# Performance work log

Measured on AMD Instinct MI355X. Metric: run time of the kernel, lower is better.

## Reference

```python
import jax, jax.numpy as jnp
import numpy as np

N_NODES = 100000
N_EDGES = 1600000
F_IN = 128
EMB = 128
HEADS = 4
D_HEAD = EMB // HEADS
HIDDEN = 256
BATCH = 2048
CANDS = 16  # distractors + 1


def setup_inputs() -> dict:
    key = jax.random.key(0)
    ks = jax.random.split(key, 10)
    message = jax.random.normal(ks[0], (BATCH, HIDDEN), jnp.float32)
    x = jax.random.normal(ks[1], (N_NODES, F_IN), jnp.float32)
    edge_index = jax.random.randint(ks[2], (2, N_EDGES), 0, N_NODES, jnp.int64)
    indices = jax.random.randint(ks[3], (BATCH * CANDS,), 0, N_NODES, jnp.int64)
    s = 1.0 / np.sqrt(F_IN)
    W = jax.random.normal(ks[4], (F_IN, HEADS, D_HEAD), jnp.float32) * s
    att_src = jax.random.normal(ks[5], (HEADS, D_HEAD), jnp.float32) * s
    att_dst = jax.random.normal(ks[6], (HEADS, D_HEAD), jnp.float32) * s
    bias = jnp.zeros((EMB,), jnp.float32)
    fc_w = jax.random.normal(ks[7], (EMB, HIDDEN), jnp.float32) / np.sqrt(HIDDEN)
    fc_b = jnp.zeros((EMB,), jnp.float32)
    return {"message": message, "x": x, "edge_index": edge_index, "indices": indices,
            "W": W, "att_src": att_src, "att_dst": att_dst, "bias": bias,
            "fc_w": fc_w, "fc_b": fc_b}


def _gat(x, edge_index, W, att_src, att_dst, bias):
    N = x.shape[0]
    loops = jnp.arange(N, dtype=edge_index.dtype)
    src = jnp.concatenate([edge_index[0], loops])  # self-loops (PyG default)
    dst = jnp.concatenate([edge_index[1], loops])
    Wx = jnp.einsum('nf,fhd->nhd', x, W)                      # [N,H,D]
    a_s = (Wx * att_src).sum(-1)                              # [N,H]
    a_d = (Wx * att_dst).sum(-1)
    e = jax.nn.leaky_relu(a_s[src] + a_d[dst], 0.2)           # [E,H]
    m = jax.ops.segment_max(e, dst, num_segments=N)           # segment softmax
    ex = jnp.exp(e - m[dst])
    den = jax.ops.segment_sum(ex, dst, num_segments=N)
    alpha = ex / den[dst]
    out = jax.ops.segment_sum(alpha[:, :, None] * Wx[src], dst, num_segments=N)
    return out.reshape(N, -1) + bias                          # [N, H*D]


def reference(message, x, edge_index, indices, W, att_src, att_dst, bias, fc_w, fc_b):
    h = _gat(x, edge_index, W, att_src, att_dst, bias)        # [N, EMB]
    B = message.shape[0]
    emb = h[indices].reshape(B, -1, h.shape[-1])              # [B,C,EMB]
    msg = message @ fc_w.T + fc_b                             # [B,EMB]
    dots = jnp.einsum('bce,be->bc', emb, msg)                 # bmm scoring
    amax = jnp.abs(dots).max()
    tie = ((jnp.abs(dots) - amax) < 1e-10).astype(dots.dtype)
    noise = jax.random.normal(jax.random.key(42), dots.shape, dots.dtype)
    dots = dots + tie * amax * 1e-5 * noise
    return jax.nn.log_softmax(dots, axis=1)
```

## Files before the change

### kernel.cpp

```cpp
#include <hip/hip_runtime.h>
#include <stdint.h>
#include <stddef.h>

#define N_NODES 100000
#define N_EDGES 1600000
#define F_IN 128
#define EMB 128
#define HEADS 4
#define D_HEAD 32
#define HIDDEN 256
#define BATCH 2048
#define CANDS 16
#define NSLOTS 32768
#define WTROWS 144
#define STR 136

#define WX_BLOCKS 782
#define MSG_BLOCKS 256
#define EDGE_QUADS 400000
#define EDGE_BLOCKS 1563
#define MEGA_BLOCKS 2610

typedef __attribute__((ext_vector_type(8))) short v8s;
typedef __attribute__((ext_vector_type(4))) float v4f;

__device__ __forceinline__ unsigned short f2bs(float f) {
  unsigned int u = __builtin_bit_cast(unsigned int, f);
  u = (u + 0x7fffu + ((u >> 16) & 1u)) >> 16;
  return (unsigned short)u;
}
__device__ __forceinline__ float bs2f(unsigned int s) {
  unsigned int u = (s & 0xffffu) << 16;
  return __builtin_bit_cast(float, u);
}

__global__ __launch_bounds__(256) void k_prep(const float* __restrict__ W,
                                              const float* __restrict__ att_src,
                                              const float* __restrict__ att_dst,
                                              unsigned short* __restrict__ Wtp,
                                              const int* __restrict__ idx,
                                              int* __restrict__ nidx,
                                              int* __restrict__ cnt) {
  int i = blockIdx.x * 256 + threadIdx.x;
  if (i < 128 * STR) {
    int r = i / STR, c = i - r * STR;
    Wtp[i] = (c < 128) ? f2bs(W[c * 128 + r]) : (unsigned short)0;
  } else if (i < WTROWS * STR) {
    int ii = i - 128 * STR;
    int r = ii / STR, c = ii - r * STR;
    unsigned short v = 0;
    if (c < 128 && r < 8) {
      const float* att = (r < 4) ? att_src : att_dst;
      int hh = r & 3;
      float s = 0.f;
#pragma unroll
      for (int d = 0; d < 32; ++d) s += W[c * 128 + hh * 32 + d] * att[hh * 32 + d];
      v = f2bs(s);
    }
    Wtp[i] = v;
  }
  if (i < NSLOTS) {
    cnt[i] = 0;
    nidx[idx[i]] = i;
  }
}

__global__ __launch_bounds__(256) void k_mega(const float* __restrict__ x,
                                              const unsigned short* __restrict__ Wtp,
                                              unsigned short* __restrict__ Wx,
                                              float* __restrict__ a_s,
                                              float* __restrict__ a_d,
                                              const int* __restrict__ ei,
                                              const int* __restrict__ idx,
                                              const int* __restrict__ nidx,
                                              int* __restrict__ cnt,
                                              int* __restrict__ srclist,
                                              const float* __restrict__ message,
                                              const float* __restrict__ fc_w,
                                              const float* __restrict__ fc_b,
                                              float* __restrict__ msg) {
  __shared__ unsigned short smem[WTROWS * STR];
  int tid = threadIdx.x;
  int sub = blockIdx.x % 10, grp = blockIdx.x / 10;

  if (sub < 3) {
    int wxid = grp * 3 + sub;
    if (wxid >= WX_BLOCKS) return;
    unsigned short* wt = smem;
    {
      const uint4* s = (const uint4*)Wtp;
      uint4* d = (uint4*)wt;
#pragma unroll
      for (int it = 0; it < 10; ++it) {
        int i = it * 256 + tid;
        if (i < WTROWS * STR / 8) d[i] = s[i];
      }
    }
    __syncthreads();

    int w = tid >> 6, lane = tid & 63;
    int m = lane & 15, quad = lane >> 4;

    for (int chunk = 0; chunk < 2; ++chunk) {
      int rbase = wxid * 128 + chunk * 64;
      int gr = rbase + w * 16 + m;
      if (gr >= N_NODES) gr = N_NODES - 1;
      const float* xrow = x + (size_t)gr * 128;

      v8s afrag[4];
#pragma unroll
      for (int t = 0; t < 4; ++t) {
        const float4* gp = (const float4*)(xrow + t * 32 + quad * 8);
        float4 f0 = gp[0], f1 = gp[1];
        v8s a;
        a[0] = (short)f2bs(f0.x); a[1] = (short)f2bs(f0.y);
        a[2] = (short)f2bs(f0.z); a[3] = (short)f2bs(f0.w);
        a[4] = (short)f2bs(f1.x); a[5] = (short)f2bs(f1.y);
        a[6] = (short)f2bs(f1.z); a[7] = (short)f2bs(f1.w);
        afrag[t] = a;
      }

      v4f acc[9];
#pragma unroll
      for (int nt = 0; nt < 9; ++nt) {
        v4f a0 = {0.f, 0.f, 0.f, 0.f};
        const unsigned short* brow = wt + (size_t)(nt * 16 + m) * STR;
#pragma unroll
        for (int t = 0; t < 4; ++t) {
          v8s b = *(const v8s*)(brow + t * 32 + quad * 8);
          a0 = __builtin_amdgcn_mfma_f32_16x16x32_bf16(afrag[t], b, a0, 0, 0, 0);
        }
        acc[nt] = a0;
      }

#pragma unroll
      for (int r = 0; r < 4; ++r) {
        int orow = rbase + w * 16 + quad * 4 + r;
        if (orow < N_NODES) {
          if (m < 4) a_s[(size_t)orow * 4 + m] = acc[8][r];
          else if (m < 8) a_d[(size_t)orow * 4 + m - 4] = acc[8][r];
          v8s v;
#pragma unroll
          for (int nt = 0; nt < 8; ++nt) v[nt] = (short)f2bs(acc[nt][r]);
          *(v8s*)(&Wx[(size_t)orow * 128 + m * 8]) = v;
        }
      }
    }
  } else if (sub == 3) {
    int msgid = grp;
    if (msgid >= MSG_BLOCKS) return;
    float* Sm = (float*)smem;
    float* red = ((float*)smem) + 2048;
    int b0 = msgid * 8;
    for (int i = tid; i < 8 * 256; i += 256)
      Sm[i] = message[(size_t)b0 * 256 + i];
    __syncthreads();
    int e = tid & 127, half = tid >> 7;
    float acc[8];
#pragma unroll
    for (int r = 0; r < 8; ++r) acc[r] = 0.f;
    const float* wrow = fc_w + (size_t)e * 256 + half * 128;
    for (int k = 0; k < 128; k += 4) {
      float4 w4 = *(const float4*)(wrow + k);
#pragma unroll
      for (int r = 0; r < 8; ++r) {
        float4 m4 = *(const float4*)(&Sm[r * 256 + half * 128 + k]);
        acc[r] += m4.x * w4.x + m4.y * w4.y + m4.z * w4.z + m4.w * w4.w;
      }
    }
    __syncthreads();
    if (half == 0) {
#pragma unroll
      for (int r = 0; r < 8; ++r) red[r * 128 + e] = acc[r];
    }
    __syncthreads();
    if (half == 1) {
#pragma unroll
      for (int r = 0; r < 8; ++r) red[r * 128 + e] += acc[r];
    }
    __syncthreads();
    for (int i = tid; i < 1024; i += 256)
      msg[(size_t)b0 * 128 + i] = red[i] + fc_b[i & 127];
  } else {
    int scid = grp * 6 + (sub - 4);
    if (scid >= EDGE_BLOCKS) return;
    int e4 = scid * 256 + tid;
    if (e4 >= EDGE_QUADS) return;
    int base = e4 * 4;
    int4 d4 = *(const int4*)(ei + N_EDGES + base);
    int4 s4 = *(const int4*)(ei + base);
    int dst[4] = {d4.x, d4.y, d4.z, d4.w};
    int src[4] = {s4.x, s4.y, s4.z, s4.w};
    unsigned int ni[4];
#pragma unroll
    for (int j = 0; j < 4; ++j) ni[j] = (unsigned int)nidx[dst[j]];
    bool ok[4];
#pragma unroll
    for (int j = 0; j < 4; ++j) {
      unsigned int c = ni[j] < NSLOTS ? ni[j] : 0u;
      ok[j] = (ni[j] < NSLOTS) && (idx[c] == dst[j]);
    }
#pragma unroll
    for (int j = 0; j < 4; ++j) {
      if (ok[j]) {
        int pos = atomicAdd(&cnt[ni[j]], 1);
        if (pos < 64) srclist[ni[j] * 64 + pos] = src[j];
      }
    }
  }
}

__global__ __launch_bounds__(256) void k_aggscore(const float* __restrict__ a_s,
                                                  const float* __restrict__ a_d,
                                                  const unsigned short* __restrict__ Wx,
                                                  const int* __restrict__ idx,
                                                  const int* __restrict__ nidx,
                                                  const int* __restrict__ cnt,
                                                  const int* __restrict__ srclist,
                                                  const int* __restrict__ ei,
                                                  const float* __restrict__ bias,
                                                  const float* __restrict__ msg,
                                                  float* __restrict__ out) {
  __shared__ int sS[16][64];
  __shared__ float sW[16][64 * 4];
  __shared__ float sdots[16];
  int w = threadIdx.x >> 6, lane = threadIdx.x & 63;
  int q = lane >> 4, li = lane & 15;
  int wq = w * 4 + q;
  int b = blockIdx.x;
  int wid = b * 16 + wq;
  int dst = idx[wid];
  int ci = nidx[dst];
  int degRaw = cnt[ci];
  int deg = degRaw < 64 ? degRaw : 64;
  float4 ad4 = *(const float4*)(a_d + (size_t)dst * 4);
  float4 dsum = {0.f, 0.f, 0.f, 0.f};
  for (int t = li; t < deg; t += 16) {
    int sv = srclist[ci * 64 + t];
    float4 as = *(const float4*)(a_s + (size_t)sv * 4);
    float e0 = as.x + ad4.x; e0 = e0 > 0.f ? e0 : 0.2f * e0;
    float e1 = as.y + ad4.y; e1 = e1 > 0.f ? e1 : 0.2f * e1;
    float e2 = as.z + ad4.z; e2 = e2 > 0.f ? e2 : 0.2f * e2;
    float e3 = as.w + ad4.w; e3 = e3 > 0.f ? e3 : 0.2f * e3;
    float4 w4;
    w4.x = __expf(e0); w4.y = __expf(e1);
    w4.z = __expf(e2); w4.w = __expf(e3);
    sS[wq][t] = sv;
    *(float4*)(&sW[wq][t * 4]) = w4;
    dsum.x += w4.x; dsum.y += w4.y; dsum.z += w4.z; dsum.w += w4.w;
  }
  asm volatile("s_waitcnt lgkmcnt(0)" ::: "memory");

#pragma unroll
  for (int o = 8; o >= 1; o >>= 1) {
    dsum.x += __shfl_xor(dsum.x, o);
    dsum.y += __shfl_xor(dsum.y, o);
    dsum.z += __shfl_xor(dsum.z, o);
    dsum.w += __shfl_xor(dsum.w, o);
  }

  float4 as4 = *(const float4*)(a_s + (size_t)dst * 4);
  float s0 = as4.x + ad4.x; s0 = s0 > 0.f ? s0 : 0.2f * s0;
  float s1 = as4.y + ad4.y; s1 = s1 > 0.f ? s1 : 0.2f * s1;
  float s2 = as4.z + ad4.z; s2 = s2 > 0.f ? s2 : 0.2f * s2;
  float s3 = as4.w + ad4.w; s3 = s3 > 0.f ? s3 : 0.2f * s3;
  float wself[4];
  wself[0] = __expf(s0); wself[1] = __expf(s1);
  wself[2] = __expf(s2); wself[3] = __expf(s3);
  float den4[4];
  den4[0] = dsum.x + wself[0]; den4[1] = dsum.y + wself[1];
  den4[2] = dsum.z + wself[2]; den4[3] = dsum.w + wself[3];

  float acc[8];
  {
    uint4 u = *(const uint4*)(Wx + (size_t)dst * 128 + li * 8);
    acc[0] = wself[0] * bs2f(u.x); acc[1] = wself[0] * bs2f(u.x >> 16);
    acc[2] = wself[1] * bs2f(u.y); acc[3] = wself[1] * bs2f(u.y >> 16);
    acc[4] = wself[2] * bs2f(u.z); acc[5] = wself[2] * bs2f(u.z >> 16);
    acc[6] = wself[3] * bs2f(u.w); acc[7] = wself[3] * bs2f(u.w >> 16);
  }

  if (degRaw > 64) {
    den4[0] = wself[0]; den4[1] = wself[1];
    den4[2] = wself[2]; den4[3] = wself[3];
    for (int e = 0; e < N_EDGES; ++e) {
      if (ei[N_EDGES + e] == dst) {
        int sv = ei[e];
        float4 as = *(const float4*)(a_s + (size_t)sv * 4);
        float e0 = as.x + ad4.x; e0 = e0 > 0.f ? e0 : 0.2f * e0;
        float e1 = as.y + ad4.y; e1 = e1 > 0.f ? e1 : 0.2f * e1;
        float e2 = as.z + ad4.z; e2 = e2 > 0.f ? e2 : 0.2f * e2;
        float e3 = as.w + ad4.w; e3 = e3 > 0.f ? e3 : 0.2f * e3;
        float wa0 = __expf(e0), wa1 = __expf(e1);
        float wa2 = __expf(e2), wa3 = __expf(e3);
        den4[0] += wa0; den4[1] += wa1; den4[2] += wa2; den4[3] += wa3;
        uint4 u = *(const uint4*)(Wx + (size_t)sv * 128 + li * 8);
        acc[0] += wa0 * bs2f(u.x); acc[1] += wa0 * bs2f(u.x >> 16);
        acc[2] += wa1 * bs2f(u.y); acc[3] += wa1 * bs2f(u.y >> 16);
        acc[4] += wa2 * bs2f(u.z); acc[5] += wa2 * bs2f(u.z >> 16);
        acc[6] += wa3 * bs2f(u.w); acc[7] += wa3 * bs2f(u.w >> 16);
      }
    }
  } else {
#pragma unroll 4
    for (int j = 0; j < deg; ++j) {
      int s = sS[wq][j];
      float4 wv = *(const float4*)(&sW[wq][j * 4]);
      uint4 u = *(const uint4*)(Wx + (size_t)s * 128 + li * 8);
      acc[0] += wv.x * bs2f(u.x); acc[1] += wv.x * bs2f(u.x >> 16);
      acc[2] += wv.y * bs2f(u.y); acc[3] += wv.y * bs2f(u.y >> 16);
      acc[4] += wv.z * bs2f(u.z); acc[5] += wv.z * bs2f(u.z >> 16);
      acc[6] += wv.w * bs2f(u.w); acc[7] += wv.w * bs2f(u.w >> 16);
    }
  }

  float invh[4];
  invh[0] = 1.0f / den4[0]; invh[1] = 1.0f / den4[1];
  invh[2] = 1.0f / den4[2]; invh[3] = 1.0f / den4[3];
  const float* mrow = msg + (size_t)b * 128;
  float dp = 0.f;
#pragma unroll
  for (int k = 0; k < 8; ++k) {
    int c = k * 16 + li;
    dp += (acc[k] * invh[k >> 1] + bias[c]) * mrow[c];
  }
#pragma unroll
  for (int o = 8; o >= 1; o >>= 1) dp += __shfl_xor(dp, o);
  if (li == 0) sdots[wq] = dp;
  __syncthreads();
  if (threadIdx.x < 16) {
    float d = sdots[threadIdx.x];
    float mx = d;
#pragma unroll
    for (int o = 1; o < 16; o <<= 1) mx = fmaxf(mx, __shfl_xor(mx, o));
    float ex = __expf(d - mx);
    float sum = ex;
#pragma unroll
    for (int o = 1; o < 16; o <<= 1) sum += __shfl_xor(sum, o);
    out[b * 16 + threadIdx.x] = d - mx - __logf(sum);
  }
}

extern "C" void kernel_launch(void* const* d_in, const int* in_sizes, int n_in,
                              void* d_out, int out_size, void* d_ws, size_t ws_size,
                              hipStream_t stream) {
  (void)in_sizes; (void)n_in; (void)out_size; (void)ws_size;
  const float* message = (const float*)d_in[0];
  const float* x       = (const float*)d_in[1];
  const int*   ei      = (const int*)d_in[2];
  const int*   indices = (const int*)d_in[3];
  const float* W       = (const float*)d_in[4];
  const float* att_src = (const float*)d_in[5];
  const float* att_dst = (const float*)d_in[6];
  const float* bias    = (const float*)d_in[7];
  const float* fc_w    = (const float*)d_in[8];
  const float* fc_b    = (const float*)d_in[9];
  float* out = (float*)d_out;

  char* p = (char*)d_ws;
  auto alloc = [&](size_t bytes) -> char* {
    char* r = p;
    p += (bytes + 255) & ~(size_t)255;
    return r;
  };
  unsigned short* Wx = (unsigned short*)alloc((size_t)N_NODES * 128 * 2);
  float* a_s = (float*)alloc((size_t)N_NODES * 4 * 4);
  float* a_d = (float*)alloc((size_t)N_NODES * 4 * 4);
  unsigned short* Wtp = (unsigned short*)alloc((size_t)WTROWS * STR * 2);
  int* nidx      = (int*)alloc((size_t)N_NODES * 4);
  int* cnt       = (int*)alloc((size_t)NSLOTS * 4);
  int* srclist   = (int*)alloc((size_t)NSLOTS * 64 * 4);
  float* msg     = (float*)alloc((size_t)BATCH * 128 * 4);

  k_prep<<<128, 256, 0, stream>>>(W, att_src, att_dst, Wtp, indices, nidx, cnt);
  k_mega<<<MEGA_BLOCKS, 256, 0, stream>>>(x, Wtp, Wx, a_s, a_d, ei, indices, nidx,
                                          cnt, srclist, message, fc_w, fc_b, msg);
  k_aggscore<<<BATCH, 256, 0, stream>>>(a_s, a_d, Wx, indices, nidx, cnt, srclist,
                                        ei, bias, msg, out);
}
```

Measured before the change: 178.9 us.

## Convert mega kernel to persistent blocks with atomic work-ticket scheduling

The fused projection/scatter/message kernel now launches a fixed set of persistent blocks. Each block pulls work units from a global atomic ticket counter, and k_prep resets that counter. A block keeps the bf16 weight tile resident in shared memory across consecutive projection units, so it is reloaded only after a message unit overwrites it. This cuts block launch overhead and repeated weight-tile loads. In exchange it adds a serialized atomic plus two barriers per unit, and the per-block work order now depends on ticket arrival.

```diff
diff --git a/kernel.cpp b/kernel.cpp
--- a/kernel.cpp
+++ b/kernel.cpp
@@ -15,11 +15,12 @@
 #define WTROWS 144
 #define STR 136
 
-#define WX_BLOCKS 782
-#define MSG_BLOCKS 256
+#define WX_UNITS 782
+#define SCAT_UNITS 1563
+#define MSG_UNITS 256
+#define N_UNITS (WX_UNITS + SCAT_UNITS + MSG_UNITS)
 #define EDGE_QUADS 400000
-#define EDGE_BLOCKS 1563
-#define MEGA_BLOCKS 2610
+#define PERSIST_BLOCKS 1024
 
 typedef __attribute__((ext_vector_type(8))) short v8s;
 typedef __attribute__((ext_vector_type(4))) float v4f;
@@ -40,8 +41,10 @@
                                               unsigned short* __restrict__ Wtp,
                                               const int* __restrict__ idx,
                                               int* __restrict__ nidx,
-                                              int* __restrict__ cnt) {
+                                              int* __restrict__ cnt,
+                                              int* __restrict__ ticket) {
   int i = blockIdx.x * 256 + threadIdx.x;
+  if (i == 0) *ticket = 0;
   if (i < 128 * STR) {
     int r = i / STR, c = i - r * STR;
     Wtp[i] = (c < 128) ? f2bs(W[c * 128 + r]) : (unsigned short)0;
@@ -78,134 +81,142 @@
                                               const float* __restrict__ message,
                                               const float* __restrict__ fc_w,
                                               const float* __restrict__ fc_b,
-                                              float* __restrict__ msg) {
+                                              float* __restrict__ msg,
+                                              int* __restrict__ ticket) {
   __shared__ unsigned short smem[WTROWS * STR];
+  __shared__ int sU;
   int tid = threadIdx.x;
-  int sub = blockIdx.x % 10, grp = blockIdx.x / 10;
-
-  if (sub < 3) {
-    int wxid = grp * 3 + sub;
-    if (wxid >= WX_BLOCKS) return;
-    unsigned short* wt = smem;
-    {
-      const uint4* s = (const uint4*)Wtp;
-      uint4* d = (uint4*)wt;
-#pragma unroll
-      for (int it = 0; it < 10; ++it) {
-        int i = it * 256 + tid;
-        if (i < WTROWS * STR / 8) d[i] = s[i];
-      }
-    }
+  bool wtValid = false;
+
+  for (;;) {
+    if (tid == 0) sU = atomicAdd(ticket, 1);
     __syncthreads();
-
-    int w = tid >> 6, lane = tid & 63;
-    int m = lane & 15, quad = lane >> 4;
-
-    for (int chunk = 0; chunk < 2; ++chunk) {
-      int rbase = wxid * 128 + chunk * 64;
-      int gr = rbase + w * 16 + m;
-      if (gr >= N_NODES) gr = N_NODES - 1;
-      const float* xrow = x + (size_t)gr * 128;
-
-      v8s afrag[4];
-#pragma unroll
-      for (int t = 0; t < 4; ++t) {
-        const float4* gp = (const float4*)(xrow + t * 32 + quad * 8);
-        float4 f0 = gp[0], f1 = gp[1];
-        v8s a;
-        a[0] = (short)f2bs(f0.x); a[1] = (short)f2bs(f0.y);
-        a[2] = (short)f2bs(f0.z); a[3] = (short)f2bs(f0.w);
-        a[4] = (short)f2bs(f1.x); a[5] = (short)f2bs(f1.y);
-        a[6] = (short)f2bs(f1.z); a[7] = (short)f2bs(f1.w);
-        afrag[t] = a;
-      }
-
-      v4f acc[9];
-#pragma unroll
-      for (int nt = 0; nt < 9; ++nt) {
-        v4f a0 = {0.f, 0.f, 0.f, 0.f};
-        const unsigned short* brow = wt + (size_t)(nt * 16 + m) * STR;
+    int u = sU;
+    __syncthreads();
+    if (u >= N_UNITS) return;
+
+    if (u < WX_UNITS) {
+      unsigned short* wt = smem;
+      if (!wtValid) {
+        const uint4* s = (const uint4*)Wtp;
+        uint4* d = (uint4*)wt;
+#pragma unroll
+        for (int it = 0; it < 10; ++it) {
+          int i = it * 256 + tid;
+          if (i < WTROWS * STR / 8) d[i] = s[i];
+        }
+        __syncthreads();
+        wtValid = true;
+      }
+
+      int w = tid >> 6, lane = tid & 63;
+      int m = lane & 15, quad = lane >> 4;
+
+      for (int chunk = 0; chunk < 2; ++chunk) {
+        int rbase = u * 128 + chunk * 64;
+        int gr = rbase + w * 16 + m;
+        if (gr >= N_NODES) gr = N_NODES - 1;
+        const float* xrow = x + (size_t)gr * 128;
+
+        v8s afrag[4];
 #pragma unroll
         for (int t = 0; t < 4; ++t) {
-          v8s b = *(const v8s*)(brow + t * 32 + quad * 8);
-          a0 = __builtin_amdgcn_mfma_f32_16x16x32_bf16(afrag[t], b, a0, 0, 0, 0);
-        }
-        acc[nt] = a0;
-      }
-
-#pragma unroll
-      for (int r = 0; r < 4; ++r) {
-        int orow = rbase + w * 16 + quad * 4 + r;
-        if (orow < N_NODES) {
-          if (m < 4) a_s[(size_t)orow * 4 + m] = acc[8][r];
-          else if (m < 8) a_d[(size_t)orow * 4 + m - 4] = acc[8][r];
-          v8s v;
-#pragma unroll
-          for (int nt = 0; nt < 8; ++nt) v[nt] = (short)f2bs(acc[nt][r]);
-          *(v8s*)(&Wx[(size_t)orow * 128 + m * 8]) = v;
-        }
-      }
-    }
-  } else if (sub == 3) {
-    int msgid = grp;
-    if (msgid >= MSG_BLOCKS) return;
-    float* Sm = (float*)smem;
-    float* red = ((float*)smem) + 2048;
-    int b0 = msgid * 8;
-    for (int i = tid; i < 8 * 256; i += 256)
-      Sm[i] = message[(size_t)b0 * 256 + i];
-    __syncthreads();
-    int e = tid & 127, half = tid >> 7;
-    float acc[8];
-#pragma unroll
-    for (int r = 0; r < 8; ++r) acc[r] = 0.f;
-    const float* wrow = fc_w + (size_t)e * 256 + half * 128;
-    for (int k = 0; k < 128; k += 4) {
-      float4 w4 = *(const float4*)(wrow + k);
-#pragma unroll
-      for (int r = 0; r < 8; ++r) {
-        float4 m4 = *(const float4*)(&Sm[r * 256 + half * 128 + k]);
-        acc[r] += m4.x * w4.x + m4.y * w4.y + m4.z * w4.z + m4.w * w4.w;
-      }
-    }
-    __syncthreads();
-    if (half == 0) {
-#pragma unroll
-      for (int r = 0; r < 8; ++r) red[r * 128 + e] = acc[r];
-    }
-    __syncthreads();
-    if (half == 1) {
-#pragma unroll
-      for (int r = 0; r < 8; ++r) red[r * 128 + e] += acc[r];
-    }
-    __syncthreads();
-    for (int i = tid; i < 1024; i += 256)
-      msg[(size_t)b0 * 128 + i] = red[i] + fc_b[i & 127];
-  } else {
-    int scid = grp * 6 + (sub - 4);
-    if (scid >= EDGE_BLOCKS) return;
-    int e4 = scid * 256 + tid;
-    if (e4 >= EDGE_QUADS) return;
-    int base = e4 * 4;
-    int4 d4 = *(const int4*)(ei + N_EDGES + base);
-    int4 s4 = *(const int4*)(ei + base);
-    int dst[4] = {d4.x, d4.y, d4.z, d4.w};
-    int src[4] = {s4.x, s4.y, s4.z, s4.w};
-    unsigned int ni[4];
-#pragma unroll
-    for (int j = 0; j < 4; ++j) ni[j] = (unsigned int)nidx[dst[j]];
-    bool ok[4];
-#pragma unroll
-    for (int j = 0; j < 4; ++j) {
-      unsigned int c = ni[j] < NSLOTS ? ni[j] : 0u;
-      ok[j] = (ni[j] < NSLOTS) && (idx[c] == dst[j]);
-    }
-#pragma unroll
-    for (int j = 0; j < 4; ++j) {
-      if (ok[j]) {
-        int pos = atomicAdd(&cnt[ni[j]], 1);
-        if (pos < 64) srclist[ni[j] * 64 + pos] = src[j];
-      }
+          const float4* gp = (const float4*)(xrow + t * 32 + quad * 8);
+          float4 f0 = gp[0], f1 = gp[1];
+          v8s a;
+          a[0] = (short)f2bs(f0.x); a[1] = (short)f2bs(f0.y);
+          a[2] = (short)f2bs(f0.z); a[3] = (short)f2bs(f0.w);
+          a[4] = (short)f2bs(f1.x); a[5] = (short)f2bs(f1.y);
+          a[6] = (short)f2bs(f1.z); a[7] = (short)f2bs(f1.w);
+          afrag[t] = a;
+        }
+
+        v4f acc[9];
+#pragma unroll
+        for (int nt = 0; nt < 9; ++nt) {
+          v4f a0 = {0.f, 0.f, 0.f, 0.f};
+          const unsigned short* brow = wt + (size_t)(nt * 16 + m) * STR;
+#pragma unroll
+          for (int t = 0; t < 4; ++t) {
+            v8s b = *(const v8s*)(brow + t * 32 + quad * 8);
+            a0 = __builtin_amdgcn_mfma_f32_16x16x32_bf16(afrag[t], b, a0, 0, 0, 0);
+          }
+          acc[nt] = a0;
+        }
+
+#pragma unroll
+        for (int r = 0; r < 4; ++r) {
+          int orow = rbase + w * 16 + quad * 4 + r;
+          if (orow < N_NODES) {
+            if (m < 4) a_s[(size_t)orow * 4 + m] = acc[8][r];
+            else if (m < 8) a_d[(size_t)orow * 4 + m - 4] = acc[8][r];
+            v8s v;
+#pragma unroll
+            for (int nt = 0; nt < 8; ++nt) v[nt] = (short)f2bs(acc[nt][r]);
+            *(v8s*)(&Wx[(size_t)orow * 128 + m * 8]) = v;
+          }
+        }
+      }
+    } else if (u < WX_UNITS + SCAT_UNITS) {
+      int e4 = (u - WX_UNITS) * 256 + tid;
+      if (e4 < EDGE_QUADS) {
+        int base = e4 * 4;
+        int4 d4 = *(const int4*)(ei + N_EDGES + base);
+        int4 s4 = *(const int4*)(ei + base);
+        int dst[4] = {d4.x, d4.y, d4.z, d4.w};
+        int src[4] = {s4.x, s4.y, s4.z, s4.w};
+        unsigned int ni[4];
+#pragma unroll
+        for (int j = 0; j < 4; ++j) ni[j] = (unsigned int)nidx[dst[j]];
+        bool ok[4];
+#pragma unroll
+        for (int j = 0; j < 4; ++j) {
+          unsigned int c = ni[j] < NSLOTS ? ni[j] : 0u;
+          ok[j] = (ni[j] < NSLOTS) && (idx[c] == dst[j]);
+        }
+#pragma unroll
+        for (int j = 0; j < 4; ++j) {
+          if (ok[j]) {
+            int pos = atomicAdd(&cnt[ni[j]], 1);
+            if (pos < 64) srclist[ni[j] * 64 + pos] = src[j];
+          }
+        }
+      }
+    } else {
+      wtValid = false;
+      float* Sm = (float*)smem;
+      float* red = ((float*)smem) + 2048;
+      int b0 = (u - WX_UNITS - SCAT_UNITS) * 8;
+      for (int i = tid; i < 8 * 256; i += 256)
+        Sm[i] = message[(size_t)b0 * 256 + i];
+      __syncthreads();
+      int e = tid & 127, half = tid >> 7;
+      float acc[8];
+#pragma unroll
+      for (int r = 0; r < 8; ++r) acc[r] = 0.f;
+      const float* wrow = fc_w + (size_t)e * 256 + half * 128;
+      for (int k = 0; k < 128; k += 4) {
+        float4 w4 = *(const float4*)(wrow + k);
+#pragma unroll
+        for (int r = 0; r < 8; ++r) {
+          float4 m4 = *(const float4*)(&Sm[r * 256 + half * 128 + k]);
+          acc[r] += m4.x * w4.x + m4.y * w4.y + m4.z * w4.z + m4.w * w4.w;
+        }
+      }
+      __syncthreads();
+      if (half == 0) {
+#pragma unroll
+        for (int r = 0; r < 8; ++r) red[r * 128 + e] = acc[r];
+      }
+      __syncthreads();
+      if (half == 1) {
+#pragma unroll
+        for (int r = 0; r < 8; ++r) red[r * 128 + e] += acc[r];
+      }
+      __syncthreads();
+      for (int i = tid; i < 1024; i += 256)
+        msg[(size_t)b0 * 128 + i] = red[i] + fc_b[i & 127];
+      __syncthreads();
     }
   }
 }
@@ -371,10 +382,12 @@
   int* cnt       = (int*)alloc((size_t)NSLOTS * 4);
   int* srclist   = (int*)alloc((size_t)NSLOTS * 64 * 4);
   float* msg     = (float*)alloc((size_t)BATCH * 128 * 4);
-
-  k_prep<<<128, 256, 0, stream>>>(W, att_src, att_dst, Wtp, indices, nidx, cnt);
-  k_mega<<<MEGA_BLOCKS, 256, 0, stream>>>(x, Wtp, Wx, a_s, a_d, ei, indices, nidx,
-                                          cnt, srclist, message, fc_w, fc_b, msg);
+  int* ticket    = (int*)alloc(4);
+
+  k_prep<<<128, 256, 0, stream>>>(W, att_src, att_dst, Wtp, indices, nidx, cnt, ticket);
+  k_mega<<<PERSIST_BLOCKS, 256, 0, stream>>>(x, Wtp, Wx, a_s, a_d, ei, indices, nidx,
+                                             cnt, srclist, message, fc_w, fc_b, msg,
+                                             ticket);
   k_aggscore<<<BATCH, 256, 0, stream>>>(a_s, a_d, Wx, indices, nidx, cnt, srclist,
                                         ei, bias, msg, out);
 }
```

New measurement: 184.4 us. 3.1% more time.
